# Kernel tuning notes

Measured on AMD Instinct MI355X. Metric: run time of the kernel, lower is better.

Reference implementation:

```python
import jax, jax.numpy as jnp
import numpy as np

MAX_SOURCE_LEN = 2048
HIDDEN = 1024
HEADS = 16
NUM_BUCKETS = 32
MAX_DISTANCE = 128
LN_EPS = 1e-5


def relative_position_bucket(relative_position, num_buckets=NUM_BUCKETS, max_distance=MAX_DISTANCE):
    # Bidirectional T5-style bucketing.
    n = -relative_position
    half = num_buckets // 2
    ret = (n < 0).astype(jnp.int32) * half
    n = jnp.abs(n)
    max_exact = half // 2
    is_small = n < max_exact
    scale = (half - max_exact) / np.log(max_distance / max_exact)
    val_large = max_exact + (jnp.log(jnp.maximum(n, 1).astype(jnp.float32) / max_exact) * scale).astype(jnp.int32)
    val_large = jnp.minimum(val_large, half - 1)
    return ret + jnp.where(is_small, n.astype(jnp.int32), val_large)


def setup_inputs() -> dict:
    key = jax.random.key(0)
    ks = jax.random.split(key, 6)
    B, L = 4, 1024
    leaf_idx = jax.random.randint(ks[0], (B, L), 0, MAX_SOURCE_LEN)
    p_emb = jax.random.normal(ks[1], (MAX_SOURCE_LEN, HIDDEN), jnp.float32) * 0.02
    p_emb = p_emb.at[0].set(0.0)  # padding_idx=0
    r_emb = jax.random.normal(ks[2], (NUM_BUCKETS + 1, HEADS), jnp.float32) * 0.02
    r_emb = r_emb.at[NUM_BUCKETS].set(0.0)  # padding_idx=num_buckets
    Wq = jax.random.normal(ks[3], (HIDDEN, HIDDEN), jnp.float32) / np.sqrt(HIDDEN)
    Wk = jax.random.normal(ks[4], (HIDDEN, HIDDEN), jnp.float32) / np.sqrt(HIDDEN)
    return {
        "leaf_idx": leaf_idx,
        "p_emb": p_emb,
        "r_emb": r_emb,
        "ln_g": jnp.ones((HIDDEN,), jnp.float32),
        "ln_b": jnp.zeros((HIDDEN,), jnp.float32),
        "Wq": Wq,
        "bq": jnp.zeros((HIDDEN,), jnp.float32),
        "Wk": Wk,
        "bk": jnp.zeros((HIDDEN,), jnp.float32),
    }


def reference(leaf_idx, p_emb, r_emb, ln_g, ln_b, Wq, bq, Wk, bk):
    B, L = leaf_idx.shape
    H = r_emb.shape[1]
    d_k = p_emb.shape[1] // H

    # --- T5 relative-position bias ---
    # rel[b,i,j] = leaf[b,j] - leaf[b,i]  (matches unsqueeze(1) - unsqueeze(-1))
    rel = leaf_idx[:, None, :] - leaf_idx[:, :, None]
    bucket = relative_position_bucket(rel)
    valid = leaf_idx != 0
    pair = valid[:, None, :] & valid[:, :, None]
    bucket = jnp.where(pair, bucket, NUM_BUCKETS)
    t5_score = jnp.transpose(r_emb[bucket], (0, 3, 1, 2))  # [B,H,L,L]

    # --- untied position score ---
    x = p_emb[leaf_idx]  # [B,L,D]
    mu = jnp.mean(x, axis=-1, keepdims=True)
    var = jnp.mean(jnp.square(x - mu), axis=-1, keepdims=True)
    xn = (x - mu) * jax.lax.rsqrt(var + LN_EPS) * ln_g + ln_b

    q = (xn @ Wq.T + bq).reshape(B, L, H, d_k).transpose(0, 2, 1, 3) / np.sqrt(d_k)
    k = (xn @ Wk.T + bk).reshape(B, L, H, d_k).transpose(0, 2, 1, 3)
    untied = jnp.einsum("bhid,bhjd->bhij", q, k)

    return untied + t5_score  # leaf_PE_Type == 'Merge'
```

## Files before the change

kernel.cpp:

```cpp
#include <hip/hip_runtime.h>
#include <hip/hip_bf16.h>

typedef __attribute__((ext_vector_type(8))) short short8;
typedef __attribute__((ext_vector_type(4))) float f32x4;

#define L 1024
#define D 1024
#define NHEADS 16
#define DK 64
#define NB 4

static __device__ __forceinline__ unsigned short f2bf(float f) {
  union { float f; unsigned int u; } c; c.f = f;
  unsigned int u = c.u;
  u += 0x7fffu + ((u >> 16) & 1u);
  return (unsigned short)(u >> 16);
}

static __device__ __forceinline__ void gload_lds16(const void* gsrc, void* ldst) {
  __builtin_amdgcn_global_load_lds(
      (const __attribute__((address_space(1))) void*)gsrc,
      (__attribute__((address_space(3))) void*)ldst, 16, 0, 0);
}

__global__ __launch_bounds__(256) void cast_w_kernel(const float* __restrict__ Wq,
                                                     const float* __restrict__ Wk,
                                                     unsigned short* __restrict__ w) {
  int idx = blockIdx.x * 256 + threadIdx.x;
  const float* src = (idx < 262144) ? Wq : Wk;
  int rel = (idx < 262144) ? idx : idx - 262144;
  float4 v = ((const float4*)src)[rel];
  ushort4 o;
  o.x = f2bf(v.x); o.y = f2bf(v.y); o.z = f2bf(v.z); o.w = f2bf(v.w);
  ((ushort4*)w)[idx] = o;
}

__global__ __launch_bounds__(256) void ln_gather_kernel(const int* __restrict__ leaf,
                                                        const float* __restrict__ p_emb,
                                                        const float* __restrict__ g,
                                                        const float* __restrict__ bcoef,
                                                        unsigned short* __restrict__ xn) {
  int row = blockIdx.x;
  int t = threadIdx.x;
  int lane = t & 63, w = t >> 6;
  int leafv = leaf[row];
  float4 xv = ((const float4*)(p_emb + (size_t)leafv * D))[t];
  float s  = xv.x + xv.y + xv.z + xv.w;
  float s2 = xv.x*xv.x + xv.y*xv.y + xv.z*xv.z + xv.w*xv.w;
  #pragma unroll
  for (int o = 1; o < 64; o <<= 1) {
    s  += __shfl_xor(s, o);
    s2 += __shfl_xor(s2, o);
  }
  __shared__ float red[8];
  if (lane == 0) { red[w*2] = s; red[w*2+1] = s2; }
  __syncthreads();
  float st  = red[0] + red[2] + red[4] + red[6];
  float s2t = red[1] + red[3] + red[5] + red[7];
  float mu = st * (1.0f/1024.0f);
  float var = s2t * (1.0f/1024.0f) - mu*mu;
  float rs = rsqrtf(var + 1e-5f);
  float4 gv = ((const float4*)g)[t];
  float4 bv = ((const float4*)bcoef)[t];
  ushort4 o;
  o.x = f2bf((xv.x - mu) * rs * gv.x + bv.x);
  o.y = f2bf((xv.y - mu) * rs * gv.y + bv.y);
  o.z = f2bf((xv.z - mu) * rs * gv.z + bv.z);
  o.w = f2bf((xv.w - mu) * rs * gv.w + bv.w);
  ((ushort4*)xn)[row * 256 + t] = o;
}

__global__ __launch_bounds__(256) void bucket_kernel(const int* __restrict__ leaf,
                                                     unsigned char* __restrict__ bucket) {
  int idx = blockIdx.x * 256 + threadIdx.x;
  int j = idx & 1023;
  int rest = idx >> 10;
  int i = rest & 1023;
  int b = rest >> 10;
  int li = leaf[b * L + i];
  int lj = leaf[b * L + j];
  int n = li - lj;
  int ret = 0;
  if (n < 0) { ret = 16; n = -n; }
  int val;
  if (n < 8) {
    val = n;
  } else {
    val = 8 + (int)(logf((float)n * 0.125f) * 2.8853900817779268f);
    if (val > 15) val = 15;
  }
  val += ret;
  if (li == 0 || lj == 0) val = 32;
  bucket[idx] = (unsigned char)val;
}

__global__ __launch_bounds__(256) void qk_gemm_kernel(const unsigned short* __restrict__ xn,
                                                      const unsigned short* __restrict__ wqk,
                                                      const float* __restrict__ bq,
                                                      const float* __restrict__ bk,
                                                      unsigned short* __restrict__ qws,
                                                      unsigned short* __restrict__ kws) {
  __shared__ __align__(16) unsigned short As[2][128 * 32];
  __shared__ __align__(16) unsigned short Bs[2][128 * 32];
  int t = threadIdx.x;
  int lane = t & 63, w = t >> 6;
  int wr = w >> 1, wc = w & 1;
  int m0 = blockIdx.y * 128;
  int n0 = blockIdx.x * 128;

  f32x4 acc[4][4] = {};

  auto stage = [&](int buf, int kt) {
    int k0 = kt * 32;
    #pragma unroll
    for (int r = 0; r < 2; ++r) {
      int c = t + r * 256;
      int row = c >> 2, kc = c & 3;
      gload_lds16(xn  + (size_t)(m0 + row) * D + k0 + kc * 8, &As[buf][c * 8]);
      gload_lds16(wqk + (size_t)(n0 + row) * D + k0 + kc * 8, &Bs[buf][c * 8]);
    }
  };

  stage(0, 0);
  __syncthreads();
  for (int kt = 0; kt < 32; ++kt) {
    int cur = kt & 1;
    if (kt < 31) stage(cur ^ 1, kt + 1);
    short8 a[4], b[4];
    #pragma unroll
    for (int f = 0; f < 4; ++f) {
      int arow = wr * 64 + f * 16 + (lane & 15);
      a[f] = *(const short8*)&As[cur][arow * 32 + (lane >> 4) * 8];
      int brow = wc * 64 + f * 16 + (lane & 15);
      b[f] = *(const short8*)&Bs[cur][brow * 32 + (lane >> 4) * 8];
    }
    #pragma unroll
    for (int i = 0; i < 4; ++i)
      #pragma unroll
      for (int j = 0; j < 4; ++j)
        acc[i][j] = __builtin_amdgcn_mfma_f32_16x16x32_bf16(a[i], b[j], acc[i][j], 0, 0, 0);
    __syncthreads();
  }

  bool isq = (n0 < 1024);
  const float* bias = isq ? bq : bk;
  float scale = isq ? 0.125f : 1.0f;
  unsigned short* outp = isq ? qws : kws;
  int nbase = n0 - (isq ? 0 : 1024);
  #pragma unroll
  for (int i = 0; i < 4; ++i) {
    #pragma unroll
    for (int j = 0; j < 4; ++j) {
      #pragma unroll
      for (int v = 0; v < 4; ++v) {
        int m = m0 + wr * 64 + i * 16 + (lane >> 4) * 4 + v;
        int ncol = nbase + wc * 64 + j * 16 + (lane & 15);
        float val = (acc[i][j][v] + bias[ncol]) * scale;
        int bb = m >> 10, ii = m & 1023;
        int h = ncol >> 6, k = ncol & 63;
        int bh = bb * NHEADS + h;
        size_t off = (size_t)bh * 65536 + (size_t)(ii >> 4) * 1024
                   + (size_t)(k >> 3) * 128 + (ii & 15) * 8 + (k & 7);
        outp[off] = f2bf(val);
      }
    }
  }
}

__global__ __launch_bounds__(256) void untied_kernel(const unsigned short* __restrict__ qws,
                                                     const unsigned short* __restrict__ kws,
                                                     const unsigned char* __restrict__ bucket,
                                                     const float* __restrict__ r_emb,
                                                     float* __restrict__ out) {
  __shared__ float rt[33 * 17];
  int t = threadIdx.x;
  for (int idx = t; idx < 528; idx += 256)
    rt[(idx >> 4) * 17 + (idx & 15)] = r_emb[idx];
  __syncthreads();

  int jt = blockIdx.x, it = blockIdx.y, bh = blockIdx.z;
  int b = bh >> 4, h = bh & 15;
  int lane = t & 63, w = t >> 6;
  int wr = w >> 1, wc = w & 1;
  int i0 = it * 128, j0 = jt * 128;

  const unsigned short* qb = qws + (size_t)bh * 65536;
  const unsigned short* kb = kws + (size_t)bh * 65536;

  short8 a[4][2], bf[4][2];
  #pragma unroll
  for (int f = 0; f < 4; ++f) {
    #pragma unroll
    for (int ks = 0; ks < 2; ++ks) {
      a[f][ks]  = *(const short8*)(qb + (size_t)(i0 / 16 + wr * 4 + f) * 1024 + ks * 512 + lane * 8);
      bf[f][ks] = *(const short8*)(kb + (size_t)(j0 / 16 + wc * 4 + f) * 1024 + ks * 512 + lane * 8);
    }
  }

  f32x4 acc[4][4] = {};
  #pragma unroll
  for (int ks = 0; ks < 2; ++ks)
    #pragma unroll
    for (int i = 0; i < 4; ++i)
      #pragma unroll
      for (int j = 0; j < 4; ++j)
        acc[i][j] = __builtin_amdgcn_mfma_f32_16x16x32_bf16(a[i][ks], bf[j][ks], acc[i][j], 0, 0, 0);

  const unsigned char* brow = bucket + (size_t)b * L * L;
  float* ob = out + (size_t)bh * L * L;
  const float* rth = rt + h;
  #pragma unroll
  for (int i = 0; i < 4; ++i) {
    #pragma unroll
    for (int j = 0; j < 4; ++j) {
      #pragma unroll
      for (int v = 0; v < 4; ++v) {
        int ii = i0 + wr * 64 + i * 16 + (lane >> 4) * 4 + v;
        int jj = j0 + wc * 64 + j * 16 + (lane & 15);
        int bk = brow[(size_t)ii * L + jj];
        ob[(size_t)ii * L + jj] = acc[i][j][v] + rth[bk * 17];
      }
    }
  }
}

extern "C" void kernel_launch(void* const* d_in, const int* in_sizes, int n_in,
                              void* d_out, int out_size, void* d_ws, size_t ws_size,
                              hipStream_t stream) {
  const int*   leaf  = (const int*)d_in[0];
  const float* p_emb = (const float*)d_in[1];
  const float* r_emb = (const float*)d_in[2];
  const float* ln_g  = (const float*)d_in[3];
  const float* ln_b  = (const float*)d_in[4];
  const float* Wq    = (const float*)d_in[5];
  const float* bq    = (const float*)d_in[6];
  const float* Wk    = (const float*)d_in[7];
  const float* bk    = (const float*)d_in[8];
  float* out = (float*)d_out;

  char* ws = (char*)d_ws;
  unsigned short* xn   = (unsigned short*)(ws);
  unsigned short* wqk  = (unsigned short*)(ws + (8u  << 20));
  unsigned short* qws  = (unsigned short*)(ws + (12u << 20));
  unsigned short* kws  = (unsigned short*)(ws + (20u << 20));
  unsigned char*  bckt = (unsigned char*)(ws + (28u << 20));

  cast_w_kernel<<<2048, 256, 0, stream>>>(Wq, Wk, wqk);
  ln_gather_kernel<<<4096, 256, 0, stream>>>(leaf, p_emb, ln_g, ln_b, xn);
  bucket_kernel<<<16384, 256, 0, stream>>>(leaf, bckt);
  qk_gemm_kernel<<<dim3(16, 32), 256, 0, stream>>>(xn, wqk, bq, bk, qws, kws);
  untied_kernel<<<dim3(8, 8, 64), 256, 0, stream>>>(qws, kws, bckt, r_emb, out);
}
```

Before: 111.3 us.

## Merge prep kernels, swizzle block order, stage bucket tiles in LDS

Three preprocessing kernels (weight cast, LayerNorm gather, bucket compute) are merged into one launch to cut launch overhead and inter-kernel gaps. The GEMM and untied kernels switch to 1D grids with an XCD-aware block remap, so blocks sharing data run on the same chiplet and its L2. The untied kernel loads its bucket tile into LDS with async global-to-LDS loads and an XOR swizzle, replacing scattered byte global reads in the epilogue. The merged kernel mixes heterogeneous block types, and the extra LDS may lower occupancy.

Measured after the change: 110.5 us. No clear change (-0.7%).

```diff
diff --git a/kernel.cpp b/kernel.cpp
--- a/kernel.cpp
+++ b/kernel.cpp
@@ -7,8 +7,6 @@
 #define L 1024
 #define D 1024
 #define NHEADS 16
-#define DK 64
-#define NB 4
 
 static __device__ __forceinline__ unsigned short f2bf(float f) {
   union { float f; unsigned int u; } c; c.f = f;
@@ -23,75 +21,75 @@
       (__attribute__((address_space(3))) void*)ldst, 16, 0, 0);
 }
 
-__global__ __launch_bounds__(256) void cast_w_kernel(const float* __restrict__ Wq,
-                                                     const float* __restrict__ Wk,
-                                                     unsigned short* __restrict__ w) {
-  int idx = blockIdx.x * 256 + threadIdx.x;
-  const float* src = (idx < 262144) ? Wq : Wk;
-  int rel = (idx < 262144) ? idx : idx - 262144;
-  float4 v = ((const float4*)src)[rel];
-  ushort4 o;
-  o.x = f2bf(v.x); o.y = f2bf(v.y); o.z = f2bf(v.z); o.w = f2bf(v.w);
-  ((ushort4*)w)[idx] = o;
-}
-
-__global__ __launch_bounds__(256) void ln_gather_kernel(const int* __restrict__ leaf,
-                                                        const float* __restrict__ p_emb,
-                                                        const float* __restrict__ g,
-                                                        const float* __restrict__ bcoef,
-                                                        unsigned short* __restrict__ xn) {
-  int row = blockIdx.x;
+__global__ __launch_bounds__(256) void prep_kernel(const int* __restrict__ leaf,
+                                                   const float* __restrict__ p_emb,
+                                                   const float* __restrict__ g,
+                                                   const float* __restrict__ bcoef,
+                                                   const float* __restrict__ Wq,
+                                                   const float* __restrict__ Wk,
+                                                   unsigned short* __restrict__ w,
+                                                   unsigned short* __restrict__ xn,
+                                                   unsigned char* __restrict__ bucket) {
+  int bid = blockIdx.x;
   int t = threadIdx.x;
-  int lane = t & 63, w = t >> 6;
-  int leafv = leaf[row];
-  float4 xv = ((const float4*)(p_emb + (size_t)leafv * D))[t];
-  float s  = xv.x + xv.y + xv.z + xv.w;
-  float s2 = xv.x*xv.x + xv.y*xv.y + xv.z*xv.z + xv.w*xv.w;
-  #pragma unroll
-  for (int o = 1; o < 64; o <<= 1) {
-    s  += __shfl_xor(s, o);
-    s2 += __shfl_xor(s2, o);
-  }
-  __shared__ float red[8];
-  if (lane == 0) { red[w*2] = s; red[w*2+1] = s2; }
-  __syncthreads();
-  float st  = red[0] + red[2] + red[4] + red[6];
-  float s2t = red[1] + red[3] + red[5] + red[7];
-  float mu = st * (1.0f/1024.0f);
-  float var = s2t * (1.0f/1024.0f) - mu*mu;
-  float rs = rsqrtf(var + 1e-5f);
-  float4 gv = ((const float4*)g)[t];
-  float4 bv = ((const float4*)bcoef)[t];
-  ushort4 o;
-  o.x = f2bf((xv.x - mu) * rs * gv.x + bv.x);
-  o.y = f2bf((xv.y - mu) * rs * gv.y + bv.y);
-  o.z = f2bf((xv.z - mu) * rs * gv.z + bv.z);
-  o.w = f2bf((xv.w - mu) * rs * gv.w + bv.w);
-  ((ushort4*)xn)[row * 256 + t] = o;
-}
-
-__global__ __launch_bounds__(256) void bucket_kernel(const int* __restrict__ leaf,
-                                                     unsigned char* __restrict__ bucket) {
-  int idx = blockIdx.x * 256 + threadIdx.x;
-  int j = idx & 1023;
-  int rest = idx >> 10;
-  int i = rest & 1023;
-  int b = rest >> 10;
-  int li = leaf[b * L + i];
-  int lj = leaf[b * L + j];
-  int n = li - lj;
-  int ret = 0;
-  if (n < 0) { ret = 16; n = -n; }
-  int val;
-  if (n < 8) {
-    val = n;
+  if (bid < 2048) {
+    int idx = bid * 256 + t;
+    const float* src = (idx < 262144) ? Wq : Wk;
+    int rel = (idx < 262144) ? idx : idx - 262144;
+    float4 v = ((const float4*)src)[rel];
+    ushort4 o;
+    o.x = f2bf(v.x); o.y = f2bf(v.y); o.z = f2bf(v.z); o.w = f2bf(v.w);
+    ((ushort4*)w)[idx] = o;
+  } else if (bid < 6144) {
+    int row = bid - 2048;
+    int lane = t & 63, wv = t >> 6;
+    int leafv = leaf[row];
+    float4 xv = ((const float4*)(p_emb + (size_t)leafv * D))[t];
+    float s  = xv.x + xv.y + xv.z + xv.w;
+    float s2 = xv.x*xv.x + xv.y*xv.y + xv.z*xv.z + xv.w*xv.w;
+    #pragma unroll
+    for (int o = 1; o < 64; o <<= 1) {
+      s  += __shfl_xor(s, o);
+      s2 += __shfl_xor(s2, o);
+    }
+    __shared__ float red[8];
+    if (lane == 0) { red[wv*2] = s; red[wv*2+1] = s2; }
+    __syncthreads();
+    float st  = red[0] + red[2] + red[4] + red[6];
+    float s2t = red[1] + red[3] + red[5] + red[7];
+    float mu = st * (1.0f/1024.0f);
+    float var = s2t * (1.0f/1024.0f) - mu*mu;
+    float rs = rsqrtf(var + 1e-5f);
+    float4 gv = ((const float4*)g)[t];
+    float4 bv = ((const float4*)bcoef)[t];
+    ushort4 o;
+    o.x = f2bf((xv.x - mu) * rs * gv.x + bv.x);
+    o.y = f2bf((xv.y - mu) * rs * gv.y + bv.y);
+    o.z = f2bf((xv.z - mu) * rs * gv.z + bv.z);
+    o.w = f2bf((xv.w - mu) * rs * gv.w + bv.w);
+    ((ushort4*)xn)[row * 256 + t] = o;
   } else {
-    val = 8 + (int)(logf((float)n * 0.125f) * 2.8853900817779268f);
-    if (val > 15) val = 15;
-  }
-  val += ret;
-  if (li == 0 || lj == 0) val = 32;
-  bucket[idx] = (unsigned char)val;
+    int idx = (bid - 6144) * 256 + t;
+    int j = idx & 1023;
+    int rest = idx >> 10;
+    int i = rest & 1023;
+    int b = rest >> 10;
+    int li = leaf[b * L + i];
+    int lj = leaf[b * L + j];
+    int n = li - lj;
+    int ret = 0;
+    if (n < 0) { ret = 16; n = -n; }
+    int val;
+    if (n < 8) {
+      val = n;
+    } else {
+      val = 8 + (int)(logf((float)n * 0.125f) * 2.8853900817779268f);
+      if (val > 15) val = 15;
+    }
+    val += ret;
+    if (li == 0 || lj == 0) val = 32;
+    bucket[idx] = (unsigned char)val;
+  }
 }
 
 __global__ __launch_bounds__(256) void qk_gemm_kernel(const unsigned short* __restrict__ xn,
@@ -105,8 +103,10 @@
   int t = threadIdx.x;
   int lane = t & 63, w = t >> 6;
   int wr = w >> 1, wc = w & 1;
-  int m0 = blockIdx.y * 128;
-  int n0 = blockIdx.x * 128;
+  int wg = blockIdx.x;
+  int swz = (wg & 7) * 64 + (wg >> 3);
+  int m0 = (swz >> 4) * 128;
+  int n0 = (swz & 15) * 128;
 
   f32x4 acc[4][4] = {};
 
@@ -173,16 +173,34 @@
                                                      const float* __restrict__ r_emb,
                                                      float* __restrict__ out) {
   __shared__ float rt[33 * 17];
+  __shared__ __align__(16) unsigned char bt[128 * 128];
   int t = threadIdx.x;
   for (int idx = t; idx < 528; idx += 256)
     rt[(idx >> 4) * 17 + (idx & 15)] = r_emb[idx];
-  __syncthreads();
-
-  int jt = blockIdx.x, it = blockIdx.y, bh = blockIdx.z;
-  int b = bh >> 4, h = bh & 15;
+
+  int bid = blockIdx.x;
+  int lg = (bid & 7) * 512 + (bid >> 3);
+  int h  = lg & 15;
+  int jt = (lg >> 4) & 7;
+  int it = (lg >> 7) & 7;
+  int b  = lg >> 10;
   int lane = t & 63, w = t >> 6;
   int wr = w >> 1, wc = w & 1;
   int i0 = it * 128, j0 = jt * 128;
+  int bh = b * NHEADS + h;
+
+  const unsigned char* bsrc = bucket + (size_t)b * L * L + (size_t)i0 * L + j0;
+  {
+    int l = lane;
+    #pragma unroll
+    for (int iter = 0; iter < 4; ++iter) {
+      int lofs = iter * 4096 + w * 1024 + l * 16;
+      int row = lofs >> 7;
+      int cb = (lofs >> 4) & 7;
+      int s = (row >> 2) & 3;
+      gload_lds16(bsrc + (size_t)row * L + (size_t)((cb ^ s) << 4), &bt[lofs]);
+    }
+  }
 
   const unsigned short* qb = qws + (size_t)bh * 65536;
   const unsigned short* kb = kws + (size_t)bh * 65536;
@@ -197,6 +215,8 @@
     }
   }
 
+  __syncthreads();
+
   f32x4 acc[4][4] = {};
   #pragma unroll
   for (int ks = 0; ks < 2; ++ks)
@@ -206,7 +226,6 @@
       for (int j = 0; j < 4; ++j)
         acc[i][j] = __builtin_amdgcn_mfma_f32_16x16x32_bf16(a[i][ks], bf[j][ks], acc[i][j], 0, 0, 0);
 
-  const unsigned char* brow = bucket + (size_t)b * L * L;
   float* ob = out + (size_t)bh * L * L;
   const float* rth = rt + h;
   #pragma unroll
@@ -215,10 +234,10 @@
     for (int j = 0; j < 4; ++j) {
       #pragma unroll
       for (int v = 0; v < 4; ++v) {
-        int ii = i0 + wr * 64 + i * 16 + (lane >> 4) * 4 + v;
-        int jj = j0 + wc * 64 + j * 16 + (lane & 15);
-        int bk = brow[(size_t)ii * L + jj];
-        ob[(size_t)ii * L + jj] = acc[i][j][v] + rth[bk * 17];
+        int il = wr * 64 + i * 16 + (lane >> 4) * 4 + v;
+        int jl = wc * 64 + j * 16 + (lane & 15);
+        int bk = bt[il * 128 + (jl ^ (((il >> 2) & 3) << 4))];
+        ob[(size_t)(i0 + il) * L + (j0 + jl)] = acc[i][j][v] + rth[bk * 17];
       }
     }
   }
@@ -245,9 +264,7 @@
   unsigned short* kws  = (unsigned short*)(ws + (20u << 20));
   unsigned char*  bckt = (unsigned char*)(ws + (28u << 20));
 
-  cast_w_kernel<<<2048, 256, 0, stream>>>(Wq, Wk, wqk);
-  ln_gather_kernel<<<4096, 256, 0, stream>>>(leaf, p_emb, ln_g, ln_b, xn);
-  bucket_kernel<<<16384, 256, 0, stream>>>(leaf, bckt);
-  qk_gemm_kernel<<<dim3(16, 32), 256, 0, stream>>>(xn, wqk, bq, bk, qws, kws);
-  untied_kernel<<<dim3(8, 8, 64), 256, 0, stream>>>(qws, kws, bckt, r_emb, out);
-}
+  prep_kernel<<<22528, 256, 0, stream>>>(leaf, p_emb, ln_g, ln_b, Wq, Wk, wqk, xn, bckt);
+  qk_gemm_kernel<<<512, 256, 0, stream>>>(xn, wqk, bq, bk, qws, kws);
+  untied_kernel<<<4096, 256, 0, stream>>>(qws, kws, bckt, r_emb, out);
+}
```
